# Optimization experiments

Hardware: AMD Instinct MI355X
Metric: run time of the kernel (lower is better)

The kernel has to match this reference:

```python
import jax, jax.numpy as jnp
import numpy as np

PAD_IND = 3
SOS_IND = 0
NSTEPS = 25
H = 256   # hidden_size
D = 256   # input_size (embedding dim)
L = 3     # lstm_layers


def _lstm_cell(x, h, c, Wih, Whh, bih, bhh):
    # torch LSTM gate order: i, f, g, o
    g = x @ Wih.T + bih + h @ Whh.T + bhh
    i, f, gg, o = jnp.split(g, 4, axis=-1)
    c2 = jax.nn.sigmoid(f) * c + jax.nn.sigmoid(i) * jnp.tanh(gg)
    h2 = jax.nn.sigmoid(o) * jnp.tanh(c2)
    return h2, c2


def setup_inputs() -> dict:
    key = jax.random.key(0)
    ks = jax.random.split(key, 24)
    B, T = 64, 256
    Vin, C = 32000, 32000
    s = 1.0 / np.sqrt(H)

    def u(k, shape):
        return jax.random.uniform(k, shape, jnp.float32, -s, s)

    return dict(
        x=jax.random.randint(ks[0], (B, T), 0, Vin),
        target_val=jax.random.randint(ks[1], (B, NSTEPS), 0, C),
        enc_embed=jax.random.normal(ks[2], (Vin, D), jnp.float32),
        enc_Wih=u(ks[3], (L, 4 * H, D)),
        enc_Whh=u(ks[4], (L, 4 * H, H)),
        enc_bih=u(ks[5], (L, 4 * H)),
        enc_bhh=u(ks[6], (L, 4 * H)),
        Wq=u(ks[7], (H, H)), bq=u(ks[8], (H,)),
        Wk=u(ks[9], (H, H)), bk=u(ks[10], (H,)),
        Wv=u(ks[11], (H, H)), bv=u(ks[12], (H,)),
        Wo=u(ks[13], (H, H)), bo=u(ks[14], (H,)),
        dec_embed=jax.random.normal(ks[15], (C, D), jnp.float32),
        dec_Wih0=u(ks[16], (4 * H, 2 * H)),            # decoder layer 0 input is [emb; ctx] = 2H
        dec_Wih_rest=u(ks[17], (L - 1, 4 * H, H)),
        dec_Whh=u(ks[18], (L, 4 * H, H)),
        dec_bih=u(ks[19], (L, 4 * H)),
        dec_bhh=u(ks[20], (L, 4 * H)),
        dec_W=u(ks[21], (C, H)),
        dec_b=u(ks[22], (C,)),
    )


def reference(x, target_val, enc_embed, enc_Wih, enc_Whh, enc_bih, enc_bhh,
              Wq, bq, Wk, bk, Wv, bv, Wo, bo,
              dec_embed, dec_Wih0, dec_Wih_rest, dec_Whh, dec_bih, dec_bhh,
              dec_W, dec_b):
    B, T = x.shape
    lengths = (x != PAD_IND).sum(axis=1)            # [B], emulates pack_padded_sequence
    emb = enc_embed[x]                              # [B,T,D]
    valid = (jnp.arange(T)[:, None] < lengths[None, :])[..., None]  # [T,B,1]
    h0 = jnp.zeros((L, B, H), emb.dtype)
    c0 = jnp.zeros((L, B, H), emb.dtype)

    def enc_step(carry, inp):
        h, c = carry
        xt, v = inp
        hs, cs = [], []
        z = xt
        for l in range(L):
            hl, cl = _lstm_cell(z, h[l], c[l], enc_Wih[l], enc_Whh[l], enc_bih[l], enc_bhh[l])
            hl = jnp.where(v, hl, h[l])             # freeze state past sequence length
            cl = jnp.where(v, cl, c[l])
            hs.append(hl); cs.append(cl)
            z = hl
        h = jnp.stack(hs); c = jnp.stack(cs)
        return (h, c), jnp.where(v, h[-1], 0.0)     # pad_packed pads with zeros

    (enc_h, enc_c), outs = jax.lax.scan(enc_step, (h0, c0), (jnp.swapaxes(emb, 0, 1), valid))
    enc_hiddens = jnp.swapaxes(outs, 0, 1)          # [B,T,H]

    # attention key/value projections are loop-invariant -> hoist out of decode loop
    kp = enc_hiddens @ Wk.T + bk                    # [B,T,H]
    vp = enc_hiddens @ Wv.T + bv                    # [B,T,H]
    scale = 1.0 / jnp.sqrt(jnp.asarray(H, emb.dtype))
    dec_Wih = [dec_Wih0, dec_Wih_rest[0], dec_Wih_rest[1]]
    tok0 = jnp.full((B,), SOS_IND, jnp.int32)

    def dec_step(carry, _):
        h, c, tok = carry
        e = dec_embed[tok]                          # [B,D]
        q = h.sum(axis=0) @ Wq.T + bq               # prev_state[0].sum(axis=0) -> [B,H]
        scores = jnp.einsum('bh,bth->bt', q, kp) * scale
        attn = jax.nn.softmax(scores, axis=-1)
        ctx = jnp.einsum('bt,bth->bh', attn, vp) @ Wo.T + bo
        z = jnp.concatenate([e, ctx], axis=-1)      # [B,2H]
        hs, cs = [], []
        for l in range(L):
            hl, cl = _lstm_cell(z, h[l], c[l], dec_Wih[l], dec_Whh[l], dec_bih[l], dec_bhh[l])
            hs.append(hl); cs.append(cl)
            z = hl
        h = jnp.stack(hs); c = jnp.stack(cs)
        logits = z @ dec_W.T + dec_b                # [B,C]
        tok = jnp.argmax(logits, axis=-1).astype(jnp.int32)  # greedy feedback (TF ratio = 0)
        return (h, c, tok), logits

    _, logits = jax.lax.scan(dec_step, (enc_h, enc_c, tok0), None, length=NSTEPS)  # [25,B,C]
    return jnp.swapaxes(logits, 0, 1)[:, :, None, :]  # [B,25,1,C] like the torch module
```

## Files before the change

### kernel.cpp

```cpp
#include <hip/hip_runtime.h>
#include <math.h>

#define TT    256
#define NB    64
#define HH    256
#define NSTEP 25
#define NCLS  32000
#define PADI  3
#define RING  4

__device__ __align__(16) float g_hring[3][RING][NB][HH];
__device__ __align__(16) float g_enchid[TT][NB][HH];
__device__ __align__(16) float g_kp[NB][TT][HH];
__device__ __align__(16) float g_vp[NB][TT][HH];
__device__ __align__(16) float g_cfin[3][NB][HH];
__device__ __align__(16) float g_hdec[2][3][NB][HH];
__device__ __align__(16) float g_cdec[3][NB][HH];
__device__ __align__(16) float g_z0[NB][512];
__device__ float    g_wmax[256][NB];
__device__ int      g_wmaxi[256][NB];
__device__ int      g_len[NB];
__device__ unsigned g_earr[3][64];
__device__ unsigned g_erel[3][64];

__device__ __forceinline__ float sigf(float v){ return 1.0f / (1.0f + expf(-v)); }

#define SCOPE_AG __HIP_MEMORY_SCOPE_AGENT
typedef unsigned long long u64;
__device__ __forceinline__ float2 ld2(const float* p){
  u64 v = __hip_atomic_load((const u64*)p, __ATOMIC_RELAXED, SCOPE_AG);
  float2 r; __builtin_memcpy(&r, &v, 8); return r;
}
__device__ __forceinline__ void  stc(float* p, float v){ __hip_atomic_store(p, v, __ATOMIC_RELAXED, SCOPE_AG); }
__device__ __forceinline__ unsigned ldu(const unsigned* p){ return __hip_atomic_load(p, __ATOMIC_RELAXED, SCOPE_AG); }
__device__ __forceinline__ void  stu(unsigned* p, unsigned v){ __hip_atomic_store(p, v, __ATOMIC_RELAXED, SCOPE_AG); }

#define DOT4(a_, x_, w_) (a_) += (x_).x*(w_).x + (x_).y*(w_).y + (x_).z*(w_).z + (x_).w*(w_).w

__global__ void __launch_bounds__(256) k_init(const int* __restrict__ p_x){
  const int blk = blockIdx.x, tid = threadIdx.x;
  if (blk < 192){
    int idx = blk*256 + tid;
    int l = idx >> 14, rem = idx & 16383;
    g_hring[l][RING-1][rem >> 8][rem & 255] = 0.f;
  } else {
    __shared__ int s_c[4];
    int b = blk - 192;
    int cnt = (p_x[b*TT + tid] != PADI) ? 1 : 0;
    #pragma unroll
    for (int m = 1; m < 64; m <<= 1) cnt += __shfl_xor(cnt, m);
    if ((tid & 63) == 0) s_c[tid >> 6] = cnt;
    __syncthreads();
    if (tid == 0) g_len[b] = s_c[0] + s_c[1] + s_c[2] + s_c[3];
  }
  if (blk == 0 && tid < 192){
    ((unsigned*)g_earr)[tid] = 0u;
    ((unsigned*)g_erel)[tid] = 0u;
  }
}

__global__ void __launch_bounds__(512, 1)
k_enc(const int*   __restrict__ p_x,
      const float* __restrict__ p_eemb,
      const float* __restrict__ p_eWih, const float* __restrict__ p_eWhh,
      const float* __restrict__ p_ebih, const float* __restrict__ p_ebhh)
{
  __shared__ __align__(16) float s_W[8192];
  __shared__ float s_gat[1024];
  __shared__ float s_b[16];
  __shared__ int   s_len[64];

  const int w = blockIdx.x, tid = threadIdx.x;
  const int l = w >> 6, q = w & 63;
  const int b2 = tid >> 4, j = tid & 15;
  const int ce = tid >> 6, cb = tid & 63;

  for (int fi = tid; fi < 8192; fi += 512){
    int row = fi >> 9, k = fi & 511;
    int e = row >> 2, g = row & 3;
    int wrow = g*256 + 4*q + e;
    s_W[fi] = (k < 256) ? p_eWih[((size_t)l*1024 + wrow)*256 + k]
                        : p_eWhh[((size_t)l*1024 + wrow)*256 + (k - 256)];
  }
  if (tid < 16){
    int e = tid >> 2, g = tid & 3;
    int wrow = g*256 + 4*q + e;
    s_b[tid] = p_ebih[l*1024 + wrow] + p_ebhh[l*1024 + wrow];
  }
  if (tid < 64) s_len[tid] = g_len[tid];
  float c_reg = 0.f, h_frz = 0.f;
  __syncthreads();

  const int li = (q & 3) << 4;
  for (int t = 0; t < TT; ++t){
    if (tid == 0){
      for (;;){
        bool ok = (ldu(&g_erel[l][li]) >= (unsigned)t);
        if (ok && l > 0)               ok = (ldu(&g_erel[l-1][li]) >= (unsigned)(t+1));
        if (ok && l < 2 && t >= RING)  ok = (ldu(&g_erel[l+1][li]) >= (unsigned)(t-(RING-1)));
        if (ok) break;
        __builtin_amdgcn_s_sleep(1);
      }
    }
    __syncthreads();

    float4 xin[2][4], hin[2][4];
    #pragma unroll
    for (int bb = 0; bb < 2; ++bb){
      const int batch = 2*b2 + bb;
      if (l == 0){
        const float* xs = p_eemb + (size_t)p_x[batch*TT + t]*HH;
        #pragma unroll
        for (int u = 0; u < 4; ++u) xin[bb][u] = *(const float4*)(xs + u*64 + 4*j);
      } else {
        const float* xs = &g_hring[l-1][t & (RING-1)][batch][0];
        #pragma unroll
        for (int u = 0; u < 4; ++u){
          float2 a = ld2(xs + u*64 + 4*j), c = ld2(xs + u*64 + 4*j + 2);
          xin[bb][u] = make_float4(a.x, a.y, c.x, c.y);
        }
      }
      const float* hs = &g_hring[l][(t + RING - 1) & (RING-1)][batch][0];
      #pragma unroll
      for (int u = 0; u < 4; ++u){
        float2 a = ld2(hs + u*64 + 4*j), c = ld2(hs + u*64 + 4*j + 2);
        hin[bb][u] = make_float4(a.x, a.y, c.x, c.y);
      }
    }

    float acc[16][2];
    #pragma unroll
    for (int r = 0; r < 16; ++r){ acc[r][0] = 0.f; acc[r][1] = 0.f; }
    #pragma unroll
    for (int u = 0; u < 8; ++u){
      float4 i0 = (u < 4) ? xin[0][u] : hin[0][u-4];
      float4 i1 = (u < 4) ? xin[1][u] : hin[1][u-4];
      #pragma unroll
      for (int row = 0; row < 16; ++row){
        float4 wv = *(const float4*)&s_W[row*512 + u*64 + 4*j];
        DOT4(acc[row][0], i0, wv);
        DOT4(acc[row][1], i1, wv);
      }
    }
    #pragma unroll
    for (int row = 0; row < 16; ++row){
      #pragma unroll
      for (int bb = 0; bb < 2; ++bb){
        float v = acc[row][bb];
        v += __shfl_xor(v, 1); v += __shfl_xor(v, 2);
        v += __shfl_xor(v, 4); v += __shfl_xor(v, 8);
        acc[row][bb] = v;
      }
    }
    if (j == 0){
      #pragma unroll
      for (int row = 0; row < 16; ++row){
        s_gat[row*64 + 2*b2    ] = acc[row][0];
        s_gat[row*64 + 2*b2 + 1] = acc[row][1];
      }
    }
    __syncthreads();

    if (tid < 256){
      float iv = s_gat[(ce*4+0)*64 + cb] + s_b[ce*4+0];
      float fv = s_gat[(ce*4+1)*64 + cb] + s_b[ce*4+1];
      float gv = s_gat[(ce*4+2)*64 + cb] + s_b[ce*4+2];
      float ov = s_gat[(ce*4+3)*64 + cb] + s_b[ce*4+3];
      float c2 = sigf(fv)*c_reg + sigf(iv)*tanhf(gv);
      float h2 = sigf(ov)*tanhf(c2);
      bool valid = (t < s_len[cb]);
      if (valid) c_reg = c2;
      h_frz = valid ? h2 : h_frz;
      stc(&g_hring[l][t & (RING-1)][cb][4*q + ce], h_frz);
      if (l == 2) g_enchid[t][cb][4*q + ce] = valid ? h_frz : 0.f;
    }

    asm volatile("s_waitcnt vmcnt(0)" ::: "memory");
    __syncthreads();
    if (tid == 0) stu(&g_earr[l][q], (unsigned)(t+1));
    if (q == 0 && tid < 64){
      while (!__all(ldu(&g_earr[l][tid]) >= (unsigned)(t+1)))
        __builtin_amdgcn_s_sleep(1);
      if (tid < 4) stu(&g_erel[l][tid << 4], (unsigned)(t+1));
    }
    __syncthreads();
  }
  if (tid < 256) g_cfin[l][cb][4*q + ce] = c_reg;
}

__global__ void __launch_bounds__(512)
k_kv(const float* __restrict__ p_Wk, const float* __restrict__ p_bk,
     const float* __restrict__ p_Wv, const float* __restrict__ p_bv)
{
  const int w = blockIdx.x, tid = threadIdx.x;
  {
    const int b3 = w >> 2, t0 = (w & 3) * 64;
    const int n1 = tid & 127, rq = tid >> 7;
    for (int p = 0; p < 4; ++p){
      const int n = p*128 + n1;
      const float* wrow = (n < 256) ? (p_Wk + (size_t)n*HH) : (p_Wv + (size_t)(n-256)*HH);
      const float bias  = (n < 256) ? p_bk[n] : p_bv[n-256];
      const float4* wr4 = (const float4*)wrow;
      const float* hb = &g_enchid[t0 + rq*16][b3][0];
      const float4* hr[16];
      #pragma unroll
      for (int r = 0; r < 16; ++r) hr[r] = (const float4*)(hb + (size_t)r*NB*HH);
      float a16[16];
      #pragma unroll
      for (int r = 0; r < 16; ++r) a16[r] = 0.f;
      for (int k4 = 0; k4 < 64; ++k4){
        float4 wv = wr4[k4];
        #pragma unroll
        for (int r = 0; r < 16; ++r){ float4 h4 = hr[r][k4]; DOT4(a16[r], h4, wv); }
      }
      float* orow = (n < 256) ? &g_kp[b3][t0 + rq*16][n] : &g_vp[b3][t0 + rq*16][n-256];
      #pragma unroll
      for (int r = 0; r < 16; ++r) orow[(size_t)r*HH] = a16[r] + bias;
    }
  }
  const int gidx = w*512 + tid;
  if (gidx < 49152){
    ((float*)g_cdec)[gidx] = ((const float*)g_cfin)[gidx];
    int l = gidx >> 14, rem = gidx & 16383;
    ((float*)g_hdec)[gidx] = g_hring[l][RING-1][rem >> 8][rem & 255];
  }
}

__device__ __forceinline__ void attn_body(int bA, int aslot, int tid,
    const float* p_Wq, const float* p_bq, const float* p_Wo, const float* p_bo,
    float* s_hs, float* s_q, float* s_sc, float* s_at, float* s_ctx, float* s_rv)
{
  if (tid < 256)
    s_hs[tid] = g_hdec[aslot][0][bA][tid] + g_hdec[aslot][1][bA][tid] + g_hdec[aslot][2][bA][tid];
  __syncthreads();
  if (tid < 256){
    float a = p_bq[tid];
    const float4* wr = (const float4*)(p_Wq + (size_t)tid*HH);
    #pragma unroll 8
    for (int k4 = 0; k4 < 64; ++k4){
      float4 wv = wr[k4]; float4 h4 = *(const float4*)&s_hs[k4*4]; DOT4(a, h4, wv);
    }
    s_q[tid] = a;
  }
  __syncthreads();
  if (tid < 256){
    float a = 0.f;
    const float4* kr = (const float4*)&g_kp[bA][tid][0];
    #pragma unroll 8
    for (int k4 = 0; k4 < 64; ++k4){
      float4 kv = kr[k4]; float4 q4 = *(const float4*)&s_q[k4*4]; DOT4(a, q4, kv);
    }
    s_sc[tid] = a * 0.0625f;
  }
  __syncthreads();
  {
    float sv = (tid < 256) ? s_sc[tid] : -1e38f;
    float m2 = sv;
    #pragma unroll
    for (int m = 1; m < 64; m <<= 1) m2 = fmaxf(m2, __shfl_xor(m2, m));
    if ((tid & 63) == 0 && tid < 256) s_rv[tid >> 6] = m2;
    __syncthreads();
    if (tid == 0){ float mm = s_rv[0]; for (int q2 = 1; q2 < 4; ++q2) mm = fmaxf(mm, s_rv[q2]); s_rv[0] = mm; }
    __syncthreads();
    const float mx = s_rv[0];
    float ev = (tid < 256) ? expf(sv - mx) : 0.f;
    float ss = ev;
    #pragma unroll
    for (int m = 1; m < 64; m <<= 1) ss += __shfl_xor(ss, m);
    __syncthreads();
    if ((tid & 63) == 0 && tid < 256) s_rv[tid >> 6] = ss;
    __syncthreads();
    if (tid == 0){ float t2 = 0.f; for (int q2 = 0; q2 < 4; ++q2) t2 += s_rv[q2]; s_rv[0] = t2; }
    __syncthreads();
    if (tid < 256) s_at[tid] = ev / s_rv[0];
  }
  __syncthreads();
  if (tid < 256){
    float a = 0.f;
    const float* vb = &g_vp[bA][0][tid];
    #pragma unroll 4
    for (int t4 = 0; t4 < 64; ++t4){
      float4 a4 = *(const float4*)&s_at[t4*4];
      a += a4.x*vb[(size_t)(t4*4+0)*HH] + a4.y*vb[(size_t)(t4*4+1)*HH]
         + a4.z*vb[(size_t)(t4*4+2)*HH] + a4.w*vb[(size_t)(t4*4+3)*HH];
    }
    s_ctx[tid] = a;
  }
  __syncthreads();
  if (tid < 256){
    float a = p_bo[tid];
    const float4* wr = (const float4*)(p_Wo + (size_t)tid*HH);
    #pragma unroll 8
    for (int k4 = 0; k4 < 64; ++k4){
      float4 wv = wr[k4]; float4 c4 = *(const float4*)&s_ctx[k4*4]; DOT4(a, c4, wv);
    }
    g_z0[bA][256 + tid] = a;
  }
}

__global__ void __launch_bounds__(256)
k_att(int aslot, const float* __restrict__ p_Wq, const float* __restrict__ p_bq,
      const float* __restrict__ p_Wo, const float* __restrict__ p_bo)
{
  __shared__ __align__(16) float s_hs[256], s_q[256], s_sc[256], s_at[256], s_ctx[256];
  __shared__ float s_rv[4];
  attn_body(blockIdx.x, aslot, threadIdx.x, p_Wq, p_bq, p_Wo, p_bo,
            s_hs, s_q, s_sc, s_at, s_ctx, s_rv);
}

template<int NCB>
__device__ __forceinline__ void dec_gates_p(const float* sw, const float* i0, const float* i1,
                                            const float* i2, int j, float out4[4]){
  float a0=0.f, a1=0.f, a2=0.f, a3=0.f;
  const float* ips[3] = { i0, i1, i2 };
  #pragma unroll
  for (int cb = 0; cb < NCB; ++cb){
    float2 xin[16];
    #pragma unroll
    for (int u = 0; u < 16; ++u) xin[u] = *(const float2*)(ips[cb] + u*16 + 2*j);
    #pragma unroll
    for (int u2 = 0; u2 < 8; ++u2){
      float2 pa = xin[2*u2], pb = xin[2*u2+1];
      const float* wb = &sw[(((cb*4+0)*8+j)*36) + u2*4];
      float4 w0 = *(const float4*)(wb);
      float4 w1 = *(const float4*)(wb + 288);
      float4 w2 = *(const float4*)(wb + 576);
      float4 w3 = *(const float4*)(wb + 864);
      a0 += pa.x*w0.x + pa.y*w0.y + pb.x*w0.z + pb.y*w0.w;
      a1 += pa.x*w1.x + pa.y*w1.y + pb.x*w1.z + pb.y*w1.w;
      a2 += pa.x*w2.x + pa.y*w2.y + pb.x*w2.z + pb.y*w2.w;
      a3 += pa.x*w3.x + pa.y*w3.y + pb.x*w3.z + pb.y*w3.w;
    }
  }
  #pragma unroll
  for (int m = 1; m < 8; m <<= 1){
    a0 += __shfl_xor(a0, m); a1 += __shfl_xor(a1, m);
    a2 += __shfl_xor(a2, m); a3 += __shfl_xor(a3, m);
  }
  out4[0]=a0; out4[1]=a1; out4[2]=a2; out4[3]=a3;
}

__global__ void __launch_bounds__(512)
k_bt(int st, const float* __restrict__ p_demb,
     const float* __restrict__ p_dWih0, const float* __restrict__ p_dWhh,
     const float* __restrict__ p_dbih,  const float* __restrict__ p_dbhh)
{
  __shared__ __align__(16) float s_w[3456];
  __shared__ float s_bd[4];
  __shared__ int   s_tok[64];
  const int w = blockIdx.x, tid = threadIdx.x;
  const int b = tid >> 3, j = tid & 7;
  const int slot = st & 1, nxt = slot ^ 1;
  for (int fi = tid; fi < 3072; fi += 512){
    int g = fi / 768, k = fi % 768; int row = g*256 + w;
    float v = (k < 512) ? p_dWih0[(size_t)row*512 + k]
                        : p_dWhh[(size_t)row*HH + (k - 512)];
    int cb = k >> 8, kk = k & 255;
    s_w[(((cb*4 + g)*8 + ((kk & 15) >> 1))*36) + (((kk >> 4) << 1) | (kk & 1))] = v;
  }
  if (tid < 4) s_bd[tid] = p_dbih[tid*256 + w] + p_dbhh[tid*256 + w];

  if (st > 0){
    float v = -1e38f; int idx = 0x7fffffff;
    #pragma unroll 4
    for (int i = 0; i < 32; ++i){
      int c = j*32 + i;
      float cv = g_wmax[c][b]; int ci = g_wmaxi[c][b];
      if (cv > v || (cv == v && ci < idx)){ v = cv; idx = ci; }
    }
    #pragma unroll
    for (int m = 1; m < 8; m <<= 1){
      float ov = __shfl_xor(v, m); int oi = __shfl_xor(idx, m);
      if (ov > v || (ov == v && oi < idx)){ v = ov; idx = oi; }
    }
    if (j == 0) s_tok[b] = idx;
  } else {
    if (tid < 64) s_tok[tid] = 0;
  }
  __syncthreads();

  const float* e0 = p_demb + (size_t)s_tok[b]*HH;
  float g4[4];
  dec_gates_p<3>(s_w, e0, &g_z0[b][256], &g_hdec[slot][0][b][0], j, g4);
  if (j == 0){
    float iv=g4[0]+s_bd[0], fv=g4[1]+s_bd[1], gv=g4[2]+s_bd[2], ov=g4[3]+s_bd[3];
    float c2 = sigf(fv)*g_cdec[0][b][w] + sigf(iv)*tanhf(gv);
    g_cdec[0][b][w] = c2;
    g_hdec[nxt][0][b][w] = sigf(ov)*tanhf(c2);
  }
}

__global__ void __launch_bounds__(512)
k_c(int st, const float* __restrict__ p_dWihR, const float* __restrict__ p_dWhh,
    const float* __restrict__ p_dbih, const float* __restrict__ p_dbhh)
{
  __shared__ __align__(16) float s_w[2304];
  __shared__ float s_bd[4];
  const int w = blockIdx.x, tid = threadIdx.x;
  const int b = tid >> 3, j = tid & 7;
  const int slot = st & 1, nxt = slot ^ 1;
  for (int fi = tid; fi < 2048; fi += 512){
    int g = fi / 512, k = fi % 512; int row = g*256 + w;
    float v = (k < 256) ? p_dWihR[(size_t)row*HH + k]
                        : p_dWhh[(size_t)(1024 + row)*HH + (k - 256)];
    int cb = k >> 8, kk = k & 255;
    s_w[(((cb*4 + g)*8 + ((kk & 15) >> 1))*36) + (((kk >> 4) << 1) | (kk & 1))] = v;
  }
  if (tid < 4) s_bd[tid] = p_dbih[1024 + tid*256 + w] + p_dbhh[1024 + tid*256 + w];
  __syncthreads();
  float g4[4];
  dec_gates_p<2>(s_w, &g_hdec[nxt][0][b][0], &g_hdec[slot][1][b][0], nullptr, j, g4);
  if (j == 0){
    float iv=g4[0]+s_bd[0], fv=g4[1]+s_bd[1], gv=g4[2]+s_bd[2], ov=g4[3]+s_bd[3];
    float c2 = sigf(fv)*g_cdec[1][b][w] + sigf(iv)*tanhf(gv);
    g_cdec[1][b][w] = c2;
    g_hdec[nxt][1][b][w] = sigf(ov)*tanhf(c2);
  }
}

__global__ void __launch_bounds__(512)
k_d(int st, const float* __restrict__ p_dWihR, const float* __restrict__ p_dWhh,
    const float* __restrict__ p_dbih, const float* __restrict__ p_dbhh)
{
  __shared__ __align__(16) float s_w[2304];
  __shared__ float s_bd[4];
  const int w = blockIdx.x, tid = threadIdx.x;
  const int b = tid >> 3, j = tid & 7;
  const int slot = st & 1, nxt = slot ^ 1;
  for (int fi = tid; fi < 2048; fi += 512){
    int g = fi / 512, k = fi % 512; int row = g*256 + w;
    float v = (k < 256) ? p_dWihR[(size_t)(1024 + row)*HH + k]
                        : p_dWhh[(size_t)(2048 + row)*HH + (k - 256)];
    int cb = k >> 8, kk = k & 255;
    s_w[(((cb*4 + g)*8 + ((kk & 15) >> 1))*36) + (((kk >> 4) << 1) | (kk & 1))] = v;
  }
  if (tid < 4) s_bd[tid] = p_dbih[2048 + tid*256 + w] + p_dbhh[2048 + tid*256 + w];
  __syncthreads();
  float g4[4];
  dec_gates_p<2>(s_w, &g_hdec[nxt][1][b][0], &g_hdec[slot][2][b][0], nullptr, j, g4);
  if (j == 0){
    float iv=g4[0]+s_bd[0], fv=g4[1]+s_bd[1], gv=g4[2]+s_bd[2], ov=g4[3]+s_bd[3];
    float c2 = sigf(fv)*g_cdec[2][b][w] + sigf(iv)*tanhf(gv);
    g_cdec[2][b][w] = c2;
    g_hdec[nxt][2][b][w] = sigf(ov)*tanhf(c2);
  }
}

__global__ void __launch_bounds__(512)
k_e2(int st, int aslot,
     const float* __restrict__ p_dW, const float* __restrict__ p_db,
     const float* __restrict__ p_Wq, const float* __restrict__ p_bq,
     const float* __restrict__ p_Wo, const float* __restrict__ p_bo,
     float* __restrict__ p_out)
{
  __shared__ __align__(16) float s_h2[NB*HH];
  const int w = blockIdx.x, tid = threadIdx.x;

  if (w >= 256){
    float* s_hs  = s_h2;
    float* s_q   = s_h2 + 256;
    float* s_sc  = s_h2 + 512;
    float* s_at  = s_h2 + 768;
    float* s_ctx = s_h2 + 1024;
    float* s_rv  = s_h2 + 1280;
    attn_body(w - 256, aslot, tid, p_Wq, p_bq, p_Wo, p_bo,
              s_hs, s_q, s_sc, s_at, s_ctx, s_rv);
    return;
  }

  {
    const float4* src = (const float4*)&g_hdec[aslot][2][0][0];
    float4* dst = (float4*)s_h2;
    #pragma unroll
    for (int u = 0; u < 8; ++u){ int i4 = tid + 512*u; dst[i4] = src[i4]; }
  }
  __syncthreads();

  const int cs = tid & 63, qb = tid >> 6;
  const bool ok0 = (2*cs)   < 125;
  const bool ok1 = (2*cs+1) < 125;
  const int c0 = w*125 + 2*cs, c1 = c0 + 1;
  const float4* wr0 = (const float4*)(p_dW + (size_t)(ok0 ? c0 : w*125)*HH);
  const float4* wr1 = (const float4*)(p_dW + (size_t)(ok1 ? c1 : w*125)*HH);
  const float4* zr[8];
  #pragma unroll
  for (int r = 0; r < 8; ++r) zr[r] = (const float4*)&s_h2[(qb*8 + r)*HH];
  float a0[8], a1[8];
  #pragma unroll
  for (int r = 0; r < 8; ++r){ a0[r] = 0.f; a1[r] = 0.f; }
  for (int k4 = 0; k4 < 64; ++k4){
    float4 w0 = wr0[k4], w1 = wr1[k4];
    #pragma unroll
    for (int r = 0; r < 8; ++r){
      float4 z4 = zr[r][k4];
      DOT4(a0[r], z4, w0);
      DOT4(a1[r], z4, w1);
    }
  }
  const float bias0 = ok0 ? p_db[c0] : 0.f;
  const float bias1 = ok1 ? p_db[c1] : 0.f;
  #pragma unroll
  for (int r = 0; r < 8; ++r){
    const int bb = qb*8 + r;
    float val0 = a0[r] + bias0, val1 = a1[r] + bias1;
    float* orow = p_out + ((size_t)bb*NSTEP + st)*NCLS;
    if (ok0) orow[c0] = val0;
    if (ok1) orow[c1] = val1;
    float v = ok0 ? val0 : -1e38f;
    int idx  = ok0 ? c0 : 0x7fffffff;
    if (ok1 && val1 > v){ v = val1; idx = c1; }
    #pragma unroll
    for (int m = 1; m < 64; m <<= 1){
      float ov = __shfl_xor(v, m); int oi = __shfl_xor(idx, m);
      if (ov > v || (ov == v && oi < idx)){ v = ov; idx = oi; }
    }
    if (cs == 0){ g_wmax[w][bb] = v; g_wmaxi[w][bb] = idx; }
  }
}

extern "C" void kernel_launch(void* const* d_in, const int* in_sizes, int n_in,
                              void* d_out, int out_size, void* d_ws, size_t ws_size,
                              hipStream_t stream){
  (void)in_sizes; (void)n_in; (void)out_size; (void)d_ws; (void)ws_size;
  const int*   x     = (const int*)d_in[0];
  const float* eemb  = (const float*)d_in[2];
  const float* eWih  = (const float*)d_in[3];
  const float* eWhh  = (const float*)d_in[4];
  const float* ebih  = (const float*)d_in[5];
  const float* ebhh  = (const float*)d_in[6];
  const float* Wq    = (const float*)d_in[7];
  const float* bq    = (const float*)d_in[8];
  const float* Wk    = (const float*)d_in[9];
  const float* bk    = (const float*)d_in[10];
  const float* Wv    = (const float*)d_in[11];
  const float* bv    = (const float*)d_in[12];
  const float* Wo    = (const float*)d_in[13];
  const float* bo    = (const float*)d_in[14];
  const float* demb  = (const float*)d_in[15];
  const float* dWih0 = (const float*)d_in[16];
  const float* dWihR = (const float*)d_in[17];
  const float* dWhh  = (const float*)d_in[18];
  const float* dbih  = (const float*)d_in[19];
  const float* dbhh  = (const float*)d_in[20];
  const float* dW    = (const float*)d_in[21];
  const float* db    = (const float*)d_in[22];
  float* out = (float*)d_out;

  k_init<<<dim3(256), dim3(256), 0, stream>>>(x);
  k_enc<<<dim3(192), dim3(512), 0, stream>>>(x, eemb, eWih, eWhh, ebih, ebhh);
  k_kv<<<dim3(256), dim3(512), 0, stream>>>(Wk, bk, Wv, bv);
  k_att<<<dim3(64), dim3(256), 0, stream>>>(0, Wq, bq, Wo, bo);
  for (int st = 0; st < NSTEP; ++st){
    const int aslot = (st & 1) ^ 1;
    k_bt<<<dim3(256), dim3(512), 0, stream>>>(st, demb, dWih0, dWhh, dbih, dbhh);
    k_c <<<dim3(256), dim3(512), 0, stream>>>(st, dWihR, dWhh, dbih, dbhh);
    k_d <<<dim3(256), dim3(512), 0, stream>>>(st, dWihR, dWhh, dbih, dbhh);
    k_e2<<<dim3(320), dim3(512), 0, stream>>>(st, aslot, dW, db, Wq, bq, Wo, bo, out);
  }
}
```

Measured before the change: 5.719 ms.

## Fuse three decoder LSTM layer kernels into one with a software grid barrier

Merges the per-layer decoder LSTM kernels into a single kernel. All three layers' weights are staged in shared memory, and layers are separated by a global atomic arrive/release barrier. This removes two kernel launches per decode step and their launch gaps. Layer outputs use agent-scope atomic stores and loads so they are visible across blocks. The cost is spin-wait barrier latency, a larger shared memory footprint, and reliance on all 256 blocks being co-resident. The encoder ring depth is also enlarged.

```diff
diff --git a/kernel.cpp b/kernel.cpp
--- a/kernel.cpp
+++ b/kernel.cpp
@@ -7,7 +7,7 @@
 #define NSTEP 25
 #define NCLS  32000
 #define PADI  3
-#define RING  4
+#define RING  8
 
 __device__ __align__(16) float g_hring[3][RING][NB][HH];
 __device__ __align__(16) float g_enchid[TT][NB][HH];
@@ -22,6 +22,8 @@
 __device__ int      g_len[NB];
 __device__ unsigned g_earr[3][64];
 __device__ unsigned g_erel[3][64];
+__device__ unsigned g_arrive[256];
+__device__ unsigned g_rel[256];
 
 __device__ __forceinline__ float sigf(float v){ return 1.0f / (1.0f + expf(-v)); }
 
@@ -57,6 +59,7 @@
     ((unsigned*)g_earr)[tid] = 0u;
     ((unsigned*)g_erel)[tid] = 0u;
   }
+  if (blk == 2){ g_arrive[tid] = 0u; g_rel[tid] = 0u; }
 }
 
 __global__ void __launch_bounds__(512, 1)
@@ -308,7 +311,7 @@
             s_hs, s_q, s_sc, s_at, s_ctx, s_rv);
 }
 
-template<int NCB>
+template<int NCB, int BASE>
 __device__ __forceinline__ void dec_gates_p(const float* sw, const float* i0, const float* i1,
                                             const float* i2, int j, float out4[4]){
   float a0=0.f, a1=0.f, a2=0.f, a3=0.f;
@@ -321,7 +324,7 @@
     #pragma unroll
     for (int u2 = 0; u2 < 8; ++u2){
       float2 pa = xin[2*u2], pb = xin[2*u2+1];
-      const float* wb = &sw[(((cb*4+0)*8+j)*36) + u2*4];
+      const float* wb = &sw[BASE + (((cb*4+0)*8+j)*36) + u2*4];
       float4 w0 = *(const float4*)(wb);
       float4 w1 = *(const float4*)(wb + 288);
       float4 w2 = *(const float4*)(wb + 576);
@@ -340,17 +343,77 @@
   out4[0]=a0; out4[1]=a1; out4[2]=a2; out4[3]=a3;
 }
 
-__global__ void __launch_bounds__(512)
-k_bt(int st, const float* __restrict__ p_demb,
-     const float* __restrict__ p_dWih0, const float* __restrict__ p_dWhh,
-     const float* __restrict__ p_dbih,  const float* __restrict__ p_dbhh)
+template<int NCB, int BASE>
+__device__ __forceinline__ void dec_gates_c(const float* sw, const float* i0, const float* i1,
+                                            int j, float out4[4]){
+  float a0=0.f, a1=0.f, a2=0.f, a3=0.f;
+  const float* ips[2] = { i0, i1 };
+  #pragma unroll
+  for (int cb = 0; cb < NCB; ++cb){
+    float2 xin[16];
+    #pragma unroll
+    for (int u = 0; u < 16; ++u) xin[u] = ld2(ips[cb] + u*16 + 2*j);
+    #pragma unroll
+    for (int u2 = 0; u2 < 8; ++u2){
+      float2 pa = xin[2*u2], pb = xin[2*u2+1];
+      const float* wb = &sw[BASE + (((cb*4+0)*8+j)*36) + u2*4];
+      float4 w0 = *(const float4*)(wb);
+      float4 w1 = *(const float4*)(wb + 288);
+      float4 w2 = *(const float4*)(wb + 576);
+      float4 w3 = *(const float4*)(wb + 864);
+      a0 += pa.x*w0.x + pa.y*w0.y + pb.x*w0.z + pb.y*w0.w;
+      a1 += pa.x*w1.x + pa.y*w1.y + pb.x*w1.z + pb.y*w1.w;
+      a2 += pa.x*w2.x + pa.y*w2.y + pb.x*w2.z + pb.y*w2.w;
+      a3 += pa.x*w3.x + pa.y*w3.y + pb.x*w3.z + pb.y*w3.w;
+    }
+  }
+  #pragma unroll
+  for (int m = 1; m < 8; m <<= 1){
+    a0 += __shfl_xor(a0, m); a1 += __shfl_xor(a1, m);
+    a2 += __shfl_xor(a2, m); a3 += __shfl_xor(a3, m);
+  }
+  out4[0]=a0; out4[1]=a1; out4[2]=a2; out4[3]=a3;
+}
+
+__device__ __forceinline__ void gbar(int w, unsigned target){
+  asm volatile("s_waitcnt vmcnt(0)" ::: "memory");
+  __syncthreads();
+  if (threadIdx.x == 0) stu(&g_arrive[w], target);
+  if (w == 0){
+    if (threadIdx.x < 64){
+      const int i4 = threadIdx.x * 4;
+      for (;;){
+        unsigned a0 = ldu(&g_arrive[i4+0]);
+        unsigned a1 = ldu(&g_arrive[i4+1]);
+        unsigned a2 = ldu(&g_arrive[i4+2]);
+        unsigned a3 = ldu(&g_arrive[i4+3]);
+        if (__all((a0>=target) && (a1>=target) && (a2>=target) && (a3>=target))) break;
+        __builtin_amdgcn_s_sleep(1);
+      }
+      if (threadIdx.x < 16) stu(&g_rel[threadIdx.x << 4], target);
+    }
+  } else {
+    if (threadIdx.x == 0){
+      const unsigned* line = &g_rel[(w >> 4) << 4];
+      while (ldu(line) < target) __builtin_amdgcn_s_sleep(1);
+    }
+  }
+  __syncthreads();
+}
+
+__global__ void __launch_bounds__(512, 1)
+k_bcd(int st, const float* __restrict__ p_demb,
+      const float* __restrict__ p_dWih0, const float* __restrict__ p_dWihR,
+      const float* __restrict__ p_dWhh,
+      const float* __restrict__ p_dbih,  const float* __restrict__ p_dbhh)
 {
-  __shared__ __align__(16) float s_w[3456];
-  __shared__ float s_bd[4];
+  __shared__ __align__(16) float s_w[8064];
+  __shared__ float s_bd[12];
   __shared__ int   s_tok[64];
   const int w = blockIdx.x, tid = threadIdx.x;
   const int b = tid >> 3, j = tid & 7;
   const int slot = st & 1, nxt = slot ^ 1;
+
   for (int fi = tid; fi < 3072; fi += 512){
     int g = fi / 768, k = fi % 768; int row = g*256 + w;
     float v = (k < 512) ? p_dWih0[(size_t)row*512 + k]
@@ -358,7 +421,24 @@
     int cb = k >> 8, kk = k & 255;
     s_w[(((cb*4 + g)*8 + ((kk & 15) >> 1))*36) + (((kk >> 4) << 1) | (kk & 1))] = v;
   }
-  if (tid < 4) s_bd[tid] = p_dbih[tid*256 + w] + p_dbhh[tid*256 + w];
+  for (int fi = tid; fi < 2048; fi += 512){
+    int g = fi / 512, k = fi % 512; int row = g*256 + w;
+    float v = (k < 256) ? p_dWihR[(size_t)row*HH + k]
+                        : p_dWhh[(size_t)(1024 + row)*HH + (k - 256)];
+    int cb = k >> 8, kk = k & 255;
+    s_w[3456 + (((cb*4 + g)*8 + ((kk & 15) >> 1))*36) + (((kk >> 4) << 1) | (kk & 1))] = v;
+  }
+  for (int fi = tid; fi < 2048; fi += 512){
+    int g = fi / 512, k = fi % 512; int row = g*256 + w;
+    float v = (k < 256) ? p_dWihR[(size_t)(1024 + row)*HH + k]
+                        : p_dWhh[(size_t)(2048 + row)*HH + (k - 256)];
+    int cb = k >> 8, kk = k & 255;
+    s_w[5760 + (((cb*4 + g)*8 + ((kk & 15) >> 1))*36) + (((kk >> 4) << 1) | (kk & 1))] = v;
+  }
+  if (tid < 12){
+    int l = tid >> 2, g = tid & 3; int row = g*256 + w;
+    s_bd[tid] = p_dbih[l*1024 + row] + p_dbhh[l*1024 + row];
+  }
 
   if (st > 0){
     float v = -1e38f; int idx = 0x7fffffff;
@@ -379,70 +459,40 @@
   }
   __syncthreads();
 
-  const float* e0 = p_demb + (size_t)s_tok[b]*HH;
-  float g4[4];
-  dec_gates_p<3>(s_w, e0, &g_z0[b][256], &g_hdec[slot][0][b][0], j, g4);
-  if (j == 0){
-    float iv=g4[0]+s_bd[0], fv=g4[1]+s_bd[1], gv=g4[2]+s_bd[2], ov=g4[3]+s_bd[3];
-    float c2 = sigf(fv)*g_cdec[0][b][w] + sigf(iv)*tanhf(gv);
-    g_cdec[0][b][w] = c2;
-    g_hdec[nxt][0][b][w] = sigf(ov)*tanhf(c2);
-  }
-}
-
-__global__ void __launch_bounds__(512)
-k_c(int st, const float* __restrict__ p_dWihR, const float* __restrict__ p_dWhh,
-    const float* __restrict__ p_dbih, const float* __restrict__ p_dbhh)
-{
-  __shared__ __align__(16) float s_w[2304];
-  __shared__ float s_bd[4];
-  const int w = blockIdx.x, tid = threadIdx.x;
-  const int b = tid >> 3, j = tid & 7;
-  const int slot = st & 1, nxt = slot ^ 1;
-  for (int fi = tid; fi < 2048; fi += 512){
-    int g = fi / 512, k = fi % 512; int row = g*256 + w;
-    float v = (k < 256) ? p_dWihR[(size_t)row*HH + k]
-                        : p_dWhh[(size_t)(1024 + row)*HH + (k - 256)];
-    int cb = k >> 8, kk = k & 255;
-    s_w[(((cb*4 + g)*8 + ((kk & 15) >> 1))*36) + (((kk >> 4) << 1) | (kk & 1))] = v;
-  }
-  if (tid < 4) s_bd[tid] = p_dbih[1024 + tid*256 + w] + p_dbhh[1024 + tid*256 + w];
-  __syncthreads();
-  float g4[4];
-  dec_gates_p<2>(s_w, &g_hdec[nxt][0][b][0], &g_hdec[slot][1][b][0], nullptr, j, g4);
-  if (j == 0){
-    float iv=g4[0]+s_bd[0], fv=g4[1]+s_bd[1], gv=g4[2]+s_bd[2], ov=g4[3]+s_bd[3];
-    float c2 = sigf(fv)*g_cdec[1][b][w] + sigf(iv)*tanhf(gv);
-    g_cdec[1][b][w] = c2;
-    g_hdec[nxt][1][b][w] = sigf(ov)*tanhf(c2);
-  }
-}
-
-__global__ void __launch_bounds__(512)
-k_d(int st, const float* __restrict__ p_dWihR, const float* __restrict__ p_dWhh,
-    const float* __restrict__ p_dbih, const float* __restrict__ p_dbhh)
-{
-  __shared__ __align__(16) float s_w[2304];
-  __shared__ float s_bd[4];
-  const int w = blockIdx.x, tid = threadIdx.x;
-  const int b = tid >> 3, j = tid & 7;
-  const int slot = st & 1, nxt = slot ^ 1;
-  for (int fi = tid; fi < 2048; fi += 512){
-    int g = fi / 512, k = fi % 512; int row = g*256 + w;
-    float v = (k < 256) ? p_dWihR[(size_t)(1024 + row)*HH + k]
-                        : p_dWhh[(size_t)(2048 + row)*HH + (k - 256)];
-    int cb = k >> 8, kk = k & 255;
-    s_w[(((cb*4 + g)*8 + ((kk & 15) >> 1))*36) + (((kk >> 4) << 1) | (kk & 1))] = v;
-  }
-  if (tid < 4) s_bd[tid] = p_dbih[2048 + tid*256 + w] + p_dbhh[2048 + tid*256 + w];
-  __syncthreads();
-  float g4[4];
-  dec_gates_p<2>(s_w, &g_hdec[nxt][1][b][0], &g_hdec[slot][2][b][0], nullptr, j, g4);
-  if (j == 0){
-    float iv=g4[0]+s_bd[0], fv=g4[1]+s_bd[1], gv=g4[2]+s_bd[2], ov=g4[3]+s_bd[3];
-    float c2 = sigf(fv)*g_cdec[2][b][w] + sigf(iv)*tanhf(gv);
-    g_cdec[2][b][w] = c2;
-    g_hdec[nxt][2][b][w] = sigf(ov)*tanhf(c2);
+  {
+    const float* e0 = p_demb + (size_t)s_tok[b]*HH;
+    float g4[4];
+    dec_gates_p<3, 0>(s_w, e0, &g_z0[b][256], &g_hdec[slot][0][b][0], j, g4);
+    if (j == 0){
+      float iv=g4[0]+s_bd[0], fv=g4[1]+s_bd[1], gv=g4[2]+s_bd[2], ov=g4[3]+s_bd[3];
+      float c2 = sigf(fv)*g_cdec[0][b][w] + sigf(iv)*tanhf(gv);
+      g_cdec[0][b][w] = c2;
+      stc(&g_hdec[nxt][0][b][w], sigf(ov)*tanhf(c2));
+    }
+  }
+  gbar(w, (unsigned)(2*st + 1));
+
+  {
+    float g4[4];
+    dec_gates_c<2, 3456>(s_w, &g_hdec[nxt][0][b][0], &g_hdec[slot][1][b][0], j, g4);
+    if (j == 0){
+      float iv=g4[0]+s_bd[4], fv=g4[1]+s_bd[5], gv=g4[2]+s_bd[6], ov=g4[3]+s_bd[7];
+      float c2 = sigf(fv)*g_cdec[1][b][w] + sigf(iv)*tanhf(gv);
+      g_cdec[1][b][w] = c2;
+      stc(&g_hdec[nxt][1][b][w], sigf(ov)*tanhf(c2));
+    }
+  }
+  gbar(w, (unsigned)(2*st + 2));
+
+  {
+    float g4[4];
+    dec_gates_c<2, 5760>(s_w, &g_hdec[nxt][1][b][0], &g_hdec[slot][2][b][0], j, g4);
+    if (j == 0){
+      float iv=g4[0]+s_bd[8], fv=g4[1]+s_bd[9], gv=g4[2]+s_bd[10], ov=g4[3]+s_bd[11];
+      float c2 = sigf(fv)*g_cdec[2][b][w] + sigf(iv)*tanhf(gv);
+      g_cdec[2][b][w] = c2;
+      stc(&g_hdec[nxt][2][b][w], sigf(ov)*tanhf(c2));
+    }
   }
 }
 
@@ -552,9 +602,7 @@
   k_att<<<dim3(64), dim3(256), 0, stream>>>(0, Wq, bq, Wo, bo);
   for (int st = 0; st < NSTEP; ++st){
     const int aslot = (st & 1) ^ 1;
-    k_bt<<<dim3(256), dim3(512), 0, stream>>>(st, demb, dWih0, dWhh, dbih, dbhh);
-    k_c <<<dim3(256), dim3(512), 0, stream>>>(st, dWihR, dWhh, dbih, dbhh);
-    k_d <<<dim3(256), dim3(512), 0, stream>>>(st, dWihR, dWhh, dbih, dbhh);
-    k_e2<<<dim3(320), dim3(512), 0, stream>>>(st, aslot, dW, db, Wq, bq, Wo, bo, out);
-  }
-}
+    k_bcd<<<dim3(256), dim3(512), 0, stream>>>(st, demb, dWih0, dWihR, dWhh, dbih, dbhh);
+    k_e2 <<<dim3(320), dim3(512), 0, stream>>>(st, aslot, dW, db, Wq, bq, Wo, bo, out);
+  }
+}
```

New measurement: 5.808 ms. Within noise of the previous version (+1.5%).
